# Kernel tuning notes

Measured on AMD Instinct MI355X. Metric: run time of the kernel, lower is better.

The kernel has to match this reference:

```python
import jax, jax.numpy as jnp
import numpy as np

VOCAB = 256   # == tagset_size (char-level CRF)
EMB = 512
HID = 1024
H = HID // 2  # per-direction hidden
T = 4096
START = 0
STOP = 1
NEG = -10000.0


def setup_inputs() -> dict:
    key = jax.random.key(0)
    ks = jax.random.split(key, 14)
    s = 0.05
    trans = jax.random.normal(ks[12], (VOCAB, VOCAB), dtype=jnp.float32)
    trans = trans.at[START, :].set(NEG).at[:, STOP].set(NEG)
    return {
        "src": jax.random.randint(ks[0], (T, 1), 0, VOCAB),
        "lengths": T,
        "embedding": jax.random.normal(ks[1], (VOCAB, EMB), dtype=jnp.float32) * s,
        "W_ih_f": jax.random.normal(ks[2], (4 * H, EMB), dtype=jnp.float32) * s,
        "W_hh_f": jax.random.normal(ks[3], (4 * H, H), dtype=jnp.float32) * s,
        "b_ih_f": jax.random.normal(ks[4], (4 * H,), dtype=jnp.float32) * s,
        "b_hh_f": jax.random.normal(ks[5], (4 * H,), dtype=jnp.float32) * s,
        "W_ih_b": jax.random.normal(ks[6], (4 * H, EMB), dtype=jnp.float32) * s,
        "W_hh_b": jax.random.normal(ks[7], (4 * H, H), dtype=jnp.float32) * s,
        "b_ih_b": jax.random.normal(ks[8], (4 * H,), dtype=jnp.float32) * s,
        "b_hh_b": jax.random.normal(ks[9], (4 * H,), dtype=jnp.float32) * s,
        "W_tag": jax.random.normal(ks[10], (VOCAB, HID), dtype=jnp.float32) * s,
        "b_tag": jax.random.normal(ks[11], (VOCAB,), dtype=jnp.float32) * s,
        "transitions": trans,
    }


def _lstm_dir(x, W_ih, W_hh, b_ih, b_hh, reverse):
    # x: [T, B, E] -> hs: [T, B, H]. PyTorch gate order: i, f, g, o.
    Hd = W_hh.shape[1]
    h0 = jnp.zeros((x.shape[1], Hd), x.dtype)

    def step(carry, x_t):
        h, c = carry
        g = x_t @ W_ih.T + b_ih + h @ W_hh.T + b_hh
        i, f, gg, o = jnp.split(g, 4, axis=-1)
        c = jax.nn.sigmoid(f) * c + jax.nn.sigmoid(i) * jnp.tanh(gg)
        h = jax.nn.sigmoid(o) * jnp.tanh(c)
        return (h, c), h

    _, hs = jax.lax.scan(step, (h0, h0), x, reverse=reverse)
    return hs


def reference(src, lengths, embedding, W_ih_f, W_hh_f, b_ih_f, b_hh_f,
              W_ih_b, W_hh_b, b_ih_b, b_hh_b, W_tag, b_tag, transitions):
    # Embedding (dropout is identity in eval mode); batch = 1 as in the torch code.
    x = embedding[src]  # [T, 1, EMB]
    hf = _lstm_dir(x, W_ih_f, W_hh_f, b_ih_f, b_hh_f, False)
    hb = _lstm_dir(x, W_ih_b, W_hh_b, b_ih_b, b_hh_b, True)
    out = jnp.concatenate([hf, hb], axis=-1)          # [T, 1, HID]
    feats = out @ W_tag.T + b_tag                     # [T, 1, K]
    f = feats[:, 0, :]                                # [T, K]
    K = transitions.shape[0]

    fv0 = jnp.full((K,), NEG, f.dtype).at[START].set(0.0)

    def vstep(fv, feat):
        scores = fv[None, :] + transitions            # [next, prev]
        bp = jnp.argmax(scores, axis=1)
        return jnp.max(scores, axis=1) + feat, bp

    fv, bps = jax.lax.scan(vstep, fv0, f)             # bps: [T, K]
    term = fv + transitions[STOP]
    best = jnp.argmax(term)
    score = term[best]

    def bt(tag, bp):
        return bp[tag], tag

    _, path = jax.lax.scan(bt, best, bps, reverse=True)  # [T], path[t] = best tag at t
    return score, path
```

## Files before the change

### kernel.cpp

```cpp
#include <hip/hip_runtime.h>
#include <stdint.h>

#define T_LEN 4096
#define NVOC 256
#define EMBD 512
#define HID 512
#define G4 2048
#define NEGV (-10000.0f)
#define START_TAG 0
#define STOP_TAG 1
#define NPROD 32

__global__ __launch_bounds__(256) void gemm_abt(
    const float* __restrict__ A, const float* __restrict__ B,
    const float* __restrict__ bias0, const float* __restrict__ bias1,
    float* __restrict__ C, int M, int N, int K)
{
    __shared__ float As[16][65];
    __shared__ float Bs[16][65];
    int m0 = blockIdx.x * 64, n0 = blockIdx.y * 64;
    int tid = threadIdx.x;
    int lr = tid >> 2;
    int lk = (tid & 3) << 2;
    int tr = tid & 15, tc = tid >> 4;
    float acc[4][4] = {};
    for (int k0 = 0; k0 < K; k0 += 16) {
        float4 av = *(const float4*)(A + (size_t)(m0 + lr) * K + k0 + lk);
        float4 bv = *(const float4*)(B + (size_t)(n0 + lr) * K + k0 + lk);
        As[lk + 0][lr] = av.x; As[lk + 1][lr] = av.y; As[lk + 2][lr] = av.z; As[lk + 3][lr] = av.w;
        Bs[lk + 0][lr] = bv.x; Bs[lk + 1][lr] = bv.y; Bs[lk + 2][lr] = bv.z; Bs[lk + 3][lr] = bv.w;
        __syncthreads();
#pragma unroll
        for (int kk = 0; kk < 16; ++kk) {
            float a[4], b[4];
#pragma unroll
            for (int x = 0; x < 4; ++x) a[x] = As[kk][tr * 4 + x];
#pragma unroll
            for (int y = 0; y < 4; ++y) b[y] = Bs[kk][tc * 4 + y];
#pragma unroll
            for (int y = 0; y < 4; ++y)
#pragma unroll
                for (int x = 0; x < 4; ++x)
                    acc[y][x] += a[x] * b[y];
        }
        __syncthreads();
    }
#pragma unroll
    for (int y = 0; y < 4; ++y) {
        int n = n0 + tc * 4 + y;
        float bb = bias0 ? bias0[n] : 0.f;
        if (bias1) bb += bias1[n];
#pragma unroll
        for (int x = 0; x < 4; ++x)
            C[(size_t)(m0 + tr * 4 + x) * N + n] = acc[y][x] + bb;
    }
}

__device__ __forceinline__ float fast_sig(float x) {
    return __builtin_amdgcn_rcpf(1.f + __expf(-x));
}
__device__ __forceinline__ float fast_tanh(float x) {
    return 2.f * __builtin_amdgcn_rcpf(1.f + __expf(-2.f * x)) - 1.f;
}

__global__ __launch_bounds__(256) void lstm_kernel(
    const int* __restrict__ src,
    const float* __restrict__ PE_f, const float* __restrict__ PE_b,
    const float* __restrict__ Whh_f, const float* __restrict__ Whh_b,
    float* __restrict__ H, unsigned long long* __restrict__ pub)
{
    int wg  = blockIdx.x & 31;
    int dir = blockIdx.x >> 5;
    const float* PE  = dir ? PE_b : PE_f;
    const float* Whh = dir ? Whh_b : Whh_f;
    unsigned long long* mypub = pub + (size_t)dir * 1024;

    int tid = threadIdx.x;
    int r = tid >> 2, q = tid & 3;
    int g = r >> 4, u = r & 15;
    int hu0 = wg * 16;
    int grow = g * 512 + hu0 + u;

    float4 w4[32];
    const float4* wsrc = (const float4*)(Whh + (size_t)grow * 512 + q * 128);
#pragma unroll
    for (int j = 0; j < 32; ++j) w4[j] = wsrc[j];

    __shared__ __align__(16) float h_sh[4][132];
    __shared__ float gate_sh[64];
    float c_state = 0.f;

    int e0 = tid * 2;
    int pq = e0 >> 7, pj = e0 & 127;

    for (int s = 0; s < T_LEN; ++s) {
        int t = dir ? (T_LEN - 1 - s) : s;
        int st = src[t];
        float pe0 = 0.f, pe1 = 0.f, pe2 = 0.f, pe3 = 0.f;
        if (tid < 16) {
            const float* pb2 = PE + (size_t)st * G4 + hu0 + tid;
            pe0 = pb2[0]; pe1 = pb2[512]; pe2 = pb2[1024]; pe3 = pb2[1536];
        }
        if (s == 0) {
            h_sh[pq][pj] = 0.f; h_sh[pq][pj + 1] = 0.f;
        } else {
            unsigned long long* p0 = mypub + (size_t)((s - 1) & 1) * 512 + e0;
            unsigned int want = (unsigned)s;
            unsigned long long w0 = __hip_atomic_load(p0, __ATOMIC_RELAXED, __HIP_MEMORY_SCOPE_AGENT);
            while ((unsigned)(w0 >> 32) < want) {
                __builtin_amdgcn_s_sleep(1);
                w0 = __hip_atomic_load(p0, __ATOMIC_RELAXED, __HIP_MEMORY_SCOPE_AGENT);
            }
            unsigned long long w1 = __hip_atomic_load(p0 + 1, __ATOMIC_RELAXED, __HIP_MEMORY_SCOPE_AGENT);
            while ((unsigned)(w1 >> 32) < want) {
                __builtin_amdgcn_s_sleep(1);
                w1 = __hip_atomic_load(p0 + 1, __ATOMIC_RELAXED, __HIP_MEMORY_SCOPE_AGENT);
            }
            __builtin_memcpy(&h_sh[pq][pj], &w0, 4);
            __builtin_memcpy(&h_sh[pq][pj + 1], &w1, 4);
        }
        __syncthreads();

        float a0 = 0.f, a1 = 0.f, a2 = 0.f, a3 = 0.f;
        const float4* hq = (const float4*)(&h_sh[q][0]);
#pragma unroll
        for (int j = 0; j < 32; ++j) {
            float4 hv = hq[j];
            a0 += w4[j].x * hv.x; a1 += w4[j].y * hv.y;
            a2 += w4[j].z * hv.z; a3 += w4[j].w * hv.w;
        }
        float dot = (a0 + a1) + (a2 + a3);
        dot += __shfl_xor(dot, 1);
        dot += __shfl_xor(dot, 2);
        if (q == 0) gate_sh[r] = dot;
        __syncthreads();

        if (tid < 16) {
            float gi = gate_sh[tid]      + pe0;
            float gf = gate_sh[16 + tid] + pe1;
            float gg = gate_sh[32 + tid] + pe2;
            float go = gate_sh[48 + tid] + pe3;
            float si = fast_sig(gi);
            float sf = fast_sig(gf);
            float so = fast_sig(go);
            float tg = fast_tanh(gg);
            c_state = sf * c_state + si * tg;
            float hval = so * fast_tanh(c_state);
            unsigned int hb; __builtin_memcpy(&hb, &hval, 4);
            unsigned long long w = ((unsigned long long)(unsigned)(s + 1) << 32) | (unsigned long long)hb;
            __hip_atomic_store(mypub + (size_t)(s & 1) * 512 + hu0 + tid, w,
                               __ATOMIC_RELAXED, __HIP_MEMORY_SCOPE_AGENT);
            H[(size_t)t * 1024 + dir * 512 + hu0 + tid] = hval;
        }
    }
}

__global__ __launch_bounds__(1024) void viterbi_fwd_kernel(
    const float* __restrict__ feats, const float* __restrict__ trans,
    float* __restrict__ fv_all)
{
    __shared__ float fv[2][256];
    __shared__ float red[4][256];
    int tid = threadIdx.x;
    int j = tid & 255, q = tid >> 8;
    float4 Tr[16];
#pragma unroll
    for (int b = 0; b < 16; ++b)
        Tr[b] = *(const float4*)(trans + (size_t)j * 256 + q * 64 + b * 4);
    if (tid < 256) fv[0][tid] = (tid == START_TAG) ? 0.f : NEGV;
    __syncthreads();
    int p = 0;
    for (int t = 0; t < T_LEN; ++t) {
        float ft = 0.f;
        if (q == 0) ft = feats[(size_t)t * 256 + j];
        float m = -1e30f;
#pragma unroll
        for (int b = 0; b < 16; ++b) {
            float4 f4 = *(const float4*)(&fv[p][q * 64 + b * 4]);
            float s0 = f4.x + Tr[b].x, s1 = f4.y + Tr[b].y;
            float s2 = f4.z + Tr[b].z, s3 = f4.w + Tr[b].w;
            m = fmaxf(m, fmaxf(s0, s1));
            m = fmaxf(m, fmaxf(s2, s3));
        }
        red[q][j] = m;
        __syncthreads();
        if (tid < 256) {
            float mm = fmaxf(fmaxf(red[0][j], red[1][j]), fmaxf(red[2][j], red[3][j]));
            float v = mm + ft;
            fv[p ^ 1][j] = v;
            fv_all[(size_t)t * 256 + j] = v;
        }
        __syncthreads();
        p ^= 1;
    }
}

__global__ __launch_bounds__(256) void bp_kernel(
    const float* __restrict__ fv_all, const float* __restrict__ trans,
    unsigned char* __restrict__ bp)
{
    __shared__ float fp[256];
    int t = blockIdx.x;
    int j = threadIdx.x;
    fp[j] = (t == 0) ? ((j == START_TAG) ? 0.f : NEGV)
                     : fv_all[(size_t)(t - 1) * 256 + j];
    __syncthreads();
    const float* Trow = trans + (size_t)j * 256;
    float m = -1e30f; int mi = 0;
    for (int i = 0; i < 256; ++i) {
        float s = fp[i] + Trow[i];
        if (s > m) { m = s; mi = i; }
    }
    bp[(size_t)t * 256 + j] = (unsigned char)mi;
}

__global__ __launch_bounds__(256) void evol_kernel(
    const unsigned char* __restrict__ bp, unsigned char* __restrict__ evol)
{
    __shared__ unsigned char tm[256];
    __shared__ unsigned char row[256];
    int s = blockIdx.x;
    int tid = threadIdx.x;
    int t_top = s * 64 + 63;
    tm[tid] = (unsigned char)tid;
    evol[(size_t)t_top * 256 + tid] = (unsigned char)tid;
    __syncthreads();
    for (int t = t_top - 1; t >= s * 64; --t) {
        row[tid] = bp[(size_t)(t + 1) * 256 + tid];
        __syncthreads();
        unsigned char nt = row[tm[tid]];
        tm[tid] = nt;
        evol[(size_t)t * 256 + tid] = nt;
        __syncthreads();
    }
}

__global__ __launch_bounds__(256) void finalize_kernel(
    const float* __restrict__ fv_all, const float* __restrict__ trans,
    const unsigned char* __restrict__ bp, const unsigned char* __restrict__ evol,
    float* __restrict__ out)
{
    __shared__ float term[256];
    __shared__ unsigned char top[64];
    int tid = threadIdx.x;
    term[tid] = fv_all[(size_t)(T_LEN - 1) * 256 + tid] + trans[STOP_TAG * 256 + tid];
    __syncthreads();
    if (tid == 0) {
        float m = term[0]; int best = 0;
        for (int i = 1; i < 256; ++i) if (term[i] > m) { m = term[i]; best = i; }
        out[0] = m;
        int tag = best;
        top[63] = (unsigned char)tag;
        for (int s2 = 63; s2 >= 1; --s2) {
            int tb = s2 * 64;
            int pb = evol[(size_t)tb * 256 + tag];
            tag = bp[(size_t)tb * 256 + pb];
            top[s2 - 1] = (unsigned char)tag;
        }
    }
    __syncthreads();
    for (int t = tid; t < T_LEN; t += 256)
        out[1 + t] = (float)evol[(size_t)t * 256 + top[t >> 6]];
}

extern "C" void kernel_launch(void* const* d_in, const int* in_sizes, int n_in,
                              void* d_out, int out_size, void* d_ws, size_t ws_size,
                              hipStream_t stream)
{
    const int*   src     = (const int*)d_in[0];
    const float* emb     = (const float*)d_in[2];
    const float* W_ih_f  = (const float*)d_in[3];
    const float* W_hh_f  = (const float*)d_in[4];
    const float* b_ih_f  = (const float*)d_in[5];
    const float* b_hh_f  = (const float*)d_in[6];
    const float* W_ih_b  = (const float*)d_in[7];
    const float* W_hh_b  = (const float*)d_in[8];
    const float* b_ih_b  = (const float*)d_in[9];
    const float* b_hh_b  = (const float*)d_in[10];
    const float* W_tag   = (const float*)d_in[11];
    const float* b_tag   = (const float*)d_in[12];
    const float* trans   = (const float*)d_in[13];
    float* out = (float*)d_out;

    char* w = (char*)d_ws;
    unsigned long long* pub = (unsigned long long*)w;
    size_t off = 16384;
    float* PE_f = (float*)(w + off); off += (size_t)NVOC * G4 * 4;
    float* PE_b = (float*)(w + off); off += (size_t)NVOC * G4 * 4;
    float* H    = (float*)(w + off); off += (size_t)T_LEN * 1024 * 4;
    float* feats= (float*)(w + off); off += (size_t)T_LEN * 256 * 4;
    float* fv   = (float*)(w + off); off += (size_t)T_LEN * 256 * 4;
    unsigned char* bp   = (unsigned char*)(w + off); off += (size_t)T_LEN * 256;
    unsigned char* evol = (unsigned char*)(w + off); off += (size_t)T_LEN * 256;

    hipMemsetAsync(pub, 0, 16384, stream);

    gemm_abt<<<dim3(NVOC / 64, G4 / 64), 256, 0, stream>>>(emb, W_ih_f, b_ih_f, b_hh_f, PE_f, NVOC, G4, EMBD);
    gemm_abt<<<dim3(NVOC / 64, G4 / 64), 256, 0, stream>>>(emb, W_ih_b, b_ih_b, b_hh_b, PE_b, NVOC, G4, EMBD);

    lstm_kernel<<<64, 256, 0, stream>>>(src, PE_f, PE_b, W_hh_f, W_hh_b, H, pub);

    gemm_abt<<<dim3(T_LEN / 64, 256 / 64), 256, 0, stream>>>(H, W_tag, b_tag, nullptr, feats, T_LEN, 256, 1024);

    viterbi_fwd_kernel<<<1, 1024, 0, stream>>>(feats, trans, fv);
    bp_kernel<<<T_LEN, 256, 0, stream>>>(fv, trans, bp);
    evol_kernel<<<T_LEN / 64, 256, 0, stream>>>(bp, evol);
    finalize_kernel<<<1, 256, 0, stream>>>(fv, trans, bp, evol, out);
}
```

Before: 10.88 ms.

## Cut per-step barriers in LSTM and Viterbi recurrences and coalesce backpointer loads

The LSTM step now double-buffers the shared hidden-state tile and gathers the four gate dot products with wave shuffles instead of a shared-memory gate array. This removes one block barrier per timestep and uses a lighter custom waitcnt+barrier. The Viterbi forward kernel reduces across its four partial maxima with shuffles (thread layout remapped), so it needs one barrier per step instead of two. The backpointer kernel reads a pre-transposed transition matrix so loads coalesce across threads, at the cost of an extra small transpose kernel and workspace buffer.

Measured after the change: 15.62 ms. 1.44x slower.

```diff
diff --git a/kernel.cpp b/kernel.cpp
--- a/kernel.cpp
+++ b/kernel.cpp
@@ -10,6 +10,11 @@
 #define START_TAG 0
 #define STOP_TAG 1
 #define NPROD 32
+
+#define BAR_LGKM() do { \
+    asm volatile("s_waitcnt lgkmcnt(0)\n\ts_barrier" ::: "memory"); \
+    __builtin_amdgcn_sched_barrier(0); \
+} while (0)
 
 __global__ __launch_bounds__(256) void gemm_abt(
     const float* __restrict__ A, const float* __restrict__ B,
@@ -76,8 +81,9 @@
     unsigned long long* mypub = pub + (size_t)dir * 1024;
 
     int tid = threadIdx.x;
-    int r = tid >> 2, q = tid & 3;
-    int g = r >> 4, u = r & 15;
+    int u = tid >> 4;
+    int g = (tid >> 2) & 3;
+    int q = tid & 3;
     int hu0 = wg * 16;
     int grow = g * 512 + hu0 + u;
 
@@ -86,43 +92,46 @@
 #pragma unroll
     for (int j = 0; j < 32; ++j) w4[j] = wsrc[j];
 
-    __shared__ __align__(16) float h_sh[4][132];
-    __shared__ float gate_sh[64];
+    __shared__ __align__(16) float h_sh[2][4][132];
     float c_state = 0.f;
+    bool leader = ((tid & 15) == 0);
 
     int e0 = tid * 2;
     int pq = e0 >> 7, pj = e0 & 127;
 
     for (int s = 0; s < T_LEN; ++s) {
+        int par = s & 1;
         int t = dir ? (T_LEN - 1 - s) : s;
         int st = src[t];
         float pe0 = 0.f, pe1 = 0.f, pe2 = 0.f, pe3 = 0.f;
-        if (tid < 16) {
-            const float* pb2 = PE + (size_t)st * G4 + hu0 + tid;
-            pe0 = pb2[0]; pe1 = pb2[512]; pe2 = pb2[1024]; pe3 = pb2[1536];
+        if (leader) {
+            const float* pb = PE + (size_t)st * G4 + hu0 + u;
+            pe0 = pb[0]; pe1 = pb[512]; pe2 = pb[1024]; pe3 = pb[1536];
         }
         if (s == 0) {
-            h_sh[pq][pj] = 0.f; h_sh[pq][pj + 1] = 0.f;
+            h_sh[0][pq][pj] = 0.f; h_sh[0][pq][pj + 1] = 0.f;
         } else {
             unsigned long long* p0 = mypub + (size_t)((s - 1) & 1) * 512 + e0;
             unsigned int want = (unsigned)s;
-            unsigned long long w0 = __hip_atomic_load(p0, __ATOMIC_RELAXED, __HIP_MEMORY_SCOPE_AGENT);
+            unsigned long long w0 = __hip_atomic_load(p0,     __ATOMIC_RELAXED, __HIP_MEMORY_SCOPE_AGENT);
+            unsigned long long w1 = __hip_atomic_load(p0 + 1, __ATOMIC_RELAXED, __HIP_MEMORY_SCOPE_AGENT);
             while ((unsigned)(w0 >> 32) < want) {
                 __builtin_amdgcn_s_sleep(1);
                 w0 = __hip_atomic_load(p0, __ATOMIC_RELAXED, __HIP_MEMORY_SCOPE_AGENT);
             }
-            unsigned long long w1 = __hip_atomic_load(p0 + 1, __ATOMIC_RELAXED, __HIP_MEMORY_SCOPE_AGENT);
             while ((unsigned)(w1 >> 32) < want) {
                 __builtin_amdgcn_s_sleep(1);
                 w1 = __hip_atomic_load(p0 + 1, __ATOMIC_RELAXED, __HIP_MEMORY_SCOPE_AGENT);
             }
-            __builtin_memcpy(&h_sh[pq][pj], &w0, 4);
-            __builtin_memcpy(&h_sh[pq][pj + 1], &w1, 4);
-        }
-        __syncthreads();
+            float f0, f1;
+            __builtin_memcpy(&f0, &w0, 4);
+            __builtin_memcpy(&f1, &w1, 4);
+            h_sh[par][pq][pj] = f0; h_sh[par][pq][pj + 1] = f1;
+        }
+        BAR_LGKM();
 
         float a0 = 0.f, a1 = 0.f, a2 = 0.f, a3 = 0.f;
-        const float4* hq = (const float4*)(&h_sh[q][0]);
+        const float4* hq = (const float4*)(&h_sh[par][q][0]);
 #pragma unroll
         for (int j = 0; j < 32; ++j) {
             float4 hv = hq[j];
@@ -132,14 +141,13 @@
         float dot = (a0 + a1) + (a2 + a3);
         dot += __shfl_xor(dot, 1);
         dot += __shfl_xor(dot, 2);
-        if (q == 0) gate_sh[r] = dot;
-        __syncthreads();
-
-        if (tid < 16) {
-            float gi = gate_sh[tid]      + pe0;
-            float gf = gate_sh[16 + tid] + pe1;
-            float gg = gate_sh[32 + tid] + pe2;
-            float go = gate_sh[48 + tid] + pe3;
+        int base = tid & ~15;
+        float di = __shfl(dot, base + 0);
+        float df = __shfl(dot, base + 4);
+        float dg = __shfl(dot, base + 8);
+        float dg_o = __shfl(dot, base + 12);
+        if (leader) {
+            float gi = di + pe0, gf = df + pe1, gg = dg + pe2, go = dg_o + pe3;
             float si = fast_sig(gi);
             float sf = fast_sig(gf);
             float so = fast_sig(go);
@@ -147,10 +155,10 @@
             c_state = sf * c_state + si * tg;
             float hval = so * fast_tanh(c_state);
             unsigned int hb; __builtin_memcpy(&hb, &hval, 4);
-            unsigned long long w = ((unsigned long long)(unsigned)(s + 1) << 32) | (unsigned long long)hb;
-            __hip_atomic_store(mypub + (size_t)(s & 1) * 512 + hu0 + tid, w,
+            unsigned long long wv = ((unsigned long long)(unsigned)(s + 1) << 32) | (unsigned long long)hb;
+            __hip_atomic_store(mypub + (size_t)par * 512 + hu0 + u, wv,
                                __ATOMIC_RELAXED, __HIP_MEMORY_SCOPE_AGENT);
-            H[(size_t)t * 1024 + dir * 512 + hu0 + tid] = hval;
+            H[(size_t)t * 1024 + dir * 512 + hu0 + u] = hval;
         }
     }
 }
@@ -160,43 +168,52 @@
     float* __restrict__ fv_all)
 {
     __shared__ float fv[2][256];
-    __shared__ float red[4][256];
-    int tid = threadIdx.x;
-    int j = tid & 255, q = tid >> 8;
+    int tid = threadIdx.x;
+    int j = tid >> 2, q = tid & 3;
     float4 Tr[16];
 #pragma unroll
     for (int b = 0; b < 16; ++b)
         Tr[b] = *(const float4*)(trans + (size_t)j * 256 + q * 64 + b * 4);
     if (tid < 256) fv[0][tid] = (tid == START_TAG) ? 0.f : NEGV;
     __syncthreads();
-    int p = 0;
     for (int t = 0; t < T_LEN; ++t) {
-        float ft = 0.f;
-        if (q == 0) ft = feats[(size_t)t * 256 + j];
-        float m = -1e30f;
+        int p = t & 1;
+        float ft = (q == 0) ? feats[(size_t)t * 256 + j] : 0.f;
+        const float4* fq = (const float4*)(&fv[p][q * 64]);
+        float m0 = -1e30f, m1 = -1e30f;
 #pragma unroll
         for (int b = 0; b < 16; ++b) {
-            float4 f4 = *(const float4*)(&fv[p][q * 64 + b * 4]);
+            float4 f4 = fq[b];
             float s0 = f4.x + Tr[b].x, s1 = f4.y + Tr[b].y;
             float s2 = f4.z + Tr[b].z, s3 = f4.w + Tr[b].w;
-            m = fmaxf(m, fmaxf(s0, s1));
-            m = fmaxf(m, fmaxf(s2, s3));
-        }
-        red[q][j] = m;
-        __syncthreads();
-        if (tid < 256) {
-            float mm = fmaxf(fmaxf(red[0][j], red[1][j]), fmaxf(red[2][j], red[3][j]));
-            float v = mm + ft;
+            m0 = fmaxf(fmaxf(m0, s0), s1);
+            m1 = fmaxf(fmaxf(m1, s2), s3);
+        }
+        float m = fmaxf(m0, m1);
+        m = fmaxf(m, __shfl_xor(m, 1));
+        m = fmaxf(m, __shfl_xor(m, 2));
+        if (q == 0) {
+            float v = m + ft;
             fv[p ^ 1][j] = v;
             fv_all[(size_t)t * 256 + j] = v;
         }
-        __syncthreads();
-        p ^= 1;
-    }
+        BAR_LGKM();
+    }
+}
+
+__global__ __launch_bounds__(256) void transpose_kernel(
+    const float* __restrict__ in, float* __restrict__ out)
+{
+    __shared__ float tile[16][17];
+    int bx = blockIdx.x & 15, by = blockIdx.x >> 4;
+    int tx = threadIdx.x & 15, ty = threadIdx.x >> 4;
+    tile[ty][tx] = in[(size_t)(by * 16 + ty) * 256 + bx * 16 + tx];
+    __syncthreads();
+    out[(size_t)(bx * 16 + ty) * 256 + by * 16 + tx] = tile[tx][ty];
 }
 
 __global__ __launch_bounds__(256) void bp_kernel(
-    const float* __restrict__ fv_all, const float* __restrict__ trans,
+    const float* __restrict__ fv_all, const float* __restrict__ transT,
     unsigned char* __restrict__ bp)
 {
     __shared__ float fp[256];
@@ -205,10 +222,10 @@
     fp[j] = (t == 0) ? ((j == START_TAG) ? 0.f : NEGV)
                      : fv_all[(size_t)(t - 1) * 256 + j];
     __syncthreads();
-    const float* Trow = trans + (size_t)j * 256;
     float m = -1e30f; int mi = 0;
+#pragma unroll 4
     for (int i = 0; i < 256; ++i) {
-        float s = fp[i] + Trow[i];
+        float s = fp[i] + transT[(size_t)i * 256 + j];
         if (s > m) { m = s; mi = i; }
     }
     bp[(size_t)t * 256 + j] = (unsigned char)mi;
@@ -290,6 +307,7 @@
     float* H    = (float*)(w + off); off += (size_t)T_LEN * 1024 * 4;
     float* feats= (float*)(w + off); off += (size_t)T_LEN * 256 * 4;
     float* fv   = (float*)(w + off); off += (size_t)T_LEN * 256 * 4;
+    float* transT = (float*)(w + off); off += (size_t)256 * 256 * 4;
     unsigned char* bp   = (unsigned char*)(w + off); off += (size_t)T_LEN * 256;
     unsigned char* evol = (unsigned char*)(w + off); off += (size_t)T_LEN * 256;
 
@@ -297,13 +315,14 @@
 
     gemm_abt<<<dim3(NVOC / 64, G4 / 64), 256, 0, stream>>>(emb, W_ih_f, b_ih_f, b_hh_f, PE_f, NVOC, G4, EMBD);
     gemm_abt<<<dim3(NVOC / 64, G4 / 64), 256, 0, stream>>>(emb, W_ih_b, b_ih_b, b_hh_b, PE_b, NVOC, G4, EMBD);
+    transpose_kernel<<<256, 256, 0, stream>>>(trans, transT);
 
     lstm_kernel<<<64, 256, 0, stream>>>(src, PE_f, PE_b, W_hh_f, W_hh_b, H, pub);
 
     gemm_abt<<<dim3(T_LEN / 64, 256 / 64), 256, 0, stream>>>(H, W_tag, b_tag, nullptr, feats, T_LEN, 256, 1024);
 
     viterbi_fwd_kernel<<<1, 1024, 0, stream>>>(feats, trans, fv);
-    bp_kernel<<<T_LEN, 256, 0, stream>>>(fv, trans, bp);
+    bp_kernel<<<T_LEN, 256, 0, stream>>>(fv, transT, bp);
     evol_kernel<<<T_LEN / 64, 256, 0, stream>>>(bp, evol);
     finalize_kernel<<<1, 256, 0, stream>>>(fv, trans, bp, evol, out);
 }
```
